# Kernel optimization log

Hardware: AMD Instinct MI355X
Metric: run time of the kernel (lower is better)

## Reference

```python
import jax, jax.numpy as jnp
import numpy as np

BIG = 1e9
EPS_BETA = 1e-6
EPS_BN = 1e-5

N_NODES = 50000
N_EDGES = 800000
IN_DIM = 128
OUT_DIM = 128


def setup_inputs() -> dict:
    key = jax.random.key(0)
    ks = jax.random.split(key, 8)
    h = jax.random.normal(ks[0], (N_NODES, IN_DIM), dtype=jnp.float32)
    src = jax.random.randint(ks[1], (N_EDGES,), 0, N_NODES, dtype=jnp.int32)
    dst = jax.random.randint(ks[2], (N_EDGES,), 0, N_NODES, dtype=jnp.int32)
    sigma_GD = jax.random.uniform(ks[3], (N_EDGES,), dtype=jnp.float32)
    fc_w = jax.random.normal(ks[4], (IN_DIM, OUT_DIM), dtype=jnp.float32) / np.sqrt(IN_DIM)
    fc_b = jax.random.normal(ks[5], (OUT_DIM,), dtype=jnp.float32) * 0.01
    attn_w = jax.random.normal(ks[6], (2 * OUT_DIM, 1), dtype=jnp.float32) / np.sqrt(2 * OUT_DIM)
    attn_b = jax.random.normal(ks[7], (1,), dtype=jnp.float32) * 0.01
    bn_gamma = jnp.ones((OUT_DIM,), dtype=jnp.float32)
    bn_beta = jnp.zeros((OUT_DIM,), dtype=jnp.float32)
    return {"h": h, "src": src, "dst": dst, "sigma_GD": sigma_GD,
            "fc_w": fc_w, "fc_b": fc_b, "attn_w": attn_w, "attn_b": attn_b,
            "bn_gamma": bn_gamma, "bn_beta": bn_beta}


def reference(h, src, dst, sigma_GD, fc_w, fc_b, attn_w, attn_b, bn_gamma, bn_beta):
    n = h.shape[0]
    # node projection
    z = h @ fc_w + fc_b                                   # [N, D]
    z = jnp.where(jnp.isinf(z), BIG, z)
    # per-edge attention logits: concat(src,dst) @ W == src@W1 + dst@W2 (avoid concat materialization)
    d = z.shape[1]
    w_src, w_dst = attn_w[:d], attn_w[d:]
    z_src = z[src]                                        # [E, D]
    a = z_src @ w_src + z[dst] @ w_dst + attn_b           # [E, 1]
    a = jnp.where(jnp.isinf(a), BIG, a)
    e = jax.nn.leaky_relu(a, negative_slope=0.01)[:, 0]   # [E]
    # segment softmax over incoming edges (mailbox softmax)
    m = jax.ops.segment_max(e, dst, num_segments=n)       # [N]
    ex = jnp.exp(e - m[dst])
    denom = jax.ops.segment_sum(ex, dst, num_segments=n)  # [N]
    alpha = ex / denom[dst]                               # [E]
    # beta: sigma_GD normalized per destination node
    bsum = jax.ops.segment_sum(sigma_GD, dst, num_segments=n)
    beta = sigma_GD / (bsum[dst] + EPS_BETA)              # [E]
    # weighted scatter-sum of source features
    h_new = jax.ops.segment_sum((alpha * beta)[:, None] * z_src, dst, num_segments=n)  # [N, D]
    h_new = jnp.where(jnp.isinf(h_new), BIG, h_new)
    # BatchNorm1d (training-mode batch stats, biased variance, as torch does)
    mu = h_new.mean(axis=0)
    var = ((h_new - mu) ** 2).mean(axis=0)
    h_bn = (h_new - mu) * jax.lax.rsqrt(var + EPS_BN) * bn_gamma + bn_beta
    return jax.nn.elu(h_bn)
```

## Files before the change

### kernel.cpp

```cpp
#include <hip/hip_runtime.h>
#include <hip/hip_fp16.h>
#include <math.h>

#define N_NODES 50000
#define N_EDGES 800000
#define BIGV 1000000000.0f
#define NBLK_SCAN 196
#define NBLK_GEMM 3125

typedef _Float16 half8 __attribute__((ext_vector_type(8)));
typedef float floatx4 __attribute__((ext_vector_type(4)));

__device__ __forceinline__ float clampinf(float x) { return isinf(x) ? BIGV : x; }

__device__ __forceinline__ void barrier_lgkm_only() {
    __builtin_amdgcn_sched_barrier(0);
    asm volatile("s_waitcnt lgkmcnt(0)" ::: "memory");
    __builtin_amdgcn_s_barrier();
    __builtin_amdgcn_sched_barrier(0);
}

__global__ __launch_bounds__(256) void k_wcast(const float* __restrict__ W,
                                               __half* __restrict__ wt,
                                               int* __restrict__ cnt,
                                               float* __restrict__ bns)
{
    int idx = blockIdx.x * 256 + threadIdx.x;
    int n = idx >> 7, k = idx & 127;
    wt[idx] = __float2half(W[k * 128 + n]);
    uint4 z; z.x = 0u; z.y = 0u; z.z = 0u; z.w = 0u;
    uint4* c4 = (uint4*)cnt;
    for (int i = idx; i < N_NODES * 4; i += 16384) c4[i] = z;
    if (idx < 256) bns[idx] = 0.f;
}

__global__ __launch_bounds__(256) void k_gemm(
    const float* __restrict__ h, const __half* __restrict__ wt,
    const float* __restrict__ bias, const float* __restrict__ attn_w,
    const int* __restrict__ dst, __half* __restrict__ zh,
    float* __restrict__ sv, float* __restrict__ tv,
    int* __restrict__ cnt, unsigned short* __restrict__ rank)
{
    __shared__ _Float16 hA[16][136];
    __shared__ float spart[4][16], tpart[4][16];

    const int tid = threadIdx.x;
    const int lane = tid & 63;
    const int wv = tid >> 6;
    const int l16 = lane & 15;
    const int oct = lane >> 4;
    const int n0 = wv << 5;
    const int node0 = blockIdx.x << 4;

    const int e = blockIdx.x * 256 + tid;
    const int d = dst[e];
    const int shard = blockIdx.x & 7;

    {
        const float4* h4 = (const float4*)(h + (size_t)node0 * 128);
        for (int i = tid; i < 512; i += 256) {
            int r = i >> 5, c4 = i & 31;
            float4 v = h4[i];
            union { __half2 h2[2]; uint2 u; } pk;
            pk.h2[0] = __floats2half2_rn(v.x, v.y);
            pk.h2[1] = __floats2half2_rn(v.z, v.w);
            *(uint2*)&hA[r][c4 << 2] = pk.u;
        }
    }

    half8 bfrag[4][2];
    #pragma unroll
    for (int kk = 0; kk < 4; ++kk)
        #pragma unroll
        for (int t = 0; t < 2; ++t)
            bfrag[kk][t] = *(const half8*)(wt + (size_t)(n0 + t * 16 + l16) * 128
                                              + kk * 32 + oct * 8);

    const float bv0 = bias[n0 + l16],         bv1 = bias[n0 + 16 + l16];
    const float ws0 = attn_w[n0 + l16],       ws1 = attn_w[n0 + 16 + l16];
    const float wd0 = attn_w[128 + n0 + l16], wd1 = attn_w[128 + n0 + 16 + l16];

    __builtin_amdgcn_sched_barrier(0);
    const int rk = atomicAdd(&cnt[(d << 4) + shard], 1);

    barrier_lgkm_only();

    floatx4 acc0 = {0.f, 0.f, 0.f, 0.f};
    floatx4 acc1 = {0.f, 0.f, 0.f, 0.f};
    #pragma unroll
    for (int kk = 0; kk < 4; ++kk) {
        half8 a = *(const half8*)&hA[l16][(kk << 5) + (oct << 3)];
        acc0 = __builtin_amdgcn_mfma_f32_16x16x32_f16(a, bfrag[kk][0], acc0, 0, 0, 0);
        acc1 = __builtin_amdgcn_mfma_f32_16x16x32_f16(a, bfrag[kk][1], acc1, 0, 0, 0);
    }

    float s_acc[4], t_acc[4];
    #pragma unroll
    for (int r = 0; r < 4; ++r) {
        float z0 = clampinf(acc0[r] + bv0);
        float z1 = clampinf(acc1[r] + bv1);
        const int row = (oct << 2) + r;
        zh[(size_t)(node0 + row) * 128 + n0 + l16]      = __float2half(z0);
        zh[(size_t)(node0 + row) * 128 + n0 + 16 + l16] = __float2half(z1);
        s_acc[r] = z0 * ws0 + z1 * ws1;
        t_acc[r] = z0 * wd0 + z1 * wd1;
    }
    #pragma unroll
    for (int r = 0; r < 4; ++r) {
        #pragma unroll
        for (int o = 1; o < 16; o <<= 1) {
            s_acc[r] += __shfl_xor(s_acc[r], o);
            t_acc[r] += __shfl_xor(t_acc[r], o);
        }
    }
    if (l16 == 0) {
        #pragma unroll
        for (int r = 0; r < 4; ++r) {
            spart[wv][(oct << 2) + r] = s_acc[r];
            tpart[wv][(oct << 2) + r] = t_acc[r];
        }
    }
    barrier_lgkm_only();
    if (tid < 16) {
        sv[node0 + tid] = spart[0][tid] + spart[1][tid] + spart[2][tid] + spart[3][tid];
        tv[node0 + tid] = tpart[0][tid] + tpart[1][tid] + tpart[2][tid] + tpart[3][tid];
    }
    rank[e] = (unsigned short)rk;
}

__global__ __launch_bounds__(256) void k_scan_bsum(int* __restrict__ cnt,
                                                   int* __restrict__ deg,
                                                   int* __restrict__ bsum)
{
    __shared__ int sdeg[256];
    const int t = threadIdx.x;
    const int idx = blockIdx.x * 256 + t;
    int dsum = 0;
    if (idx < N_NODES) {
        uint4* p = (uint4*)(cnt + ((size_t)idx << 4));
        uint4 a = p[0], b = p[1];
        unsigned e0 = 0;
        unsigned e1 = e0 + a.x;
        unsigned e2 = e1 + a.y;
        unsigned e3 = e2 + a.z;
        unsigned e4 = e3 + a.w;
        unsigned e5 = e4 + b.x;
        unsigned e6 = e5 + b.y;
        unsigned e7 = e6 + b.z;
        dsum = (int)(e7 + b.w);
        uint4 pa; pa.x = e0; pa.y = e1; pa.z = e2; pa.w = e3;
        uint4 pb; pb.x = e4; pb.y = e5; pb.z = e6; pb.w = e7;
        p[0] = pa; p[1] = pb;
        deg[idx] = dsum;
    }
    sdeg[t] = dsum;
    __syncthreads();
    for (int off = 128; off; off >>= 1) {
        if (t < off) sdeg[t] += sdeg[t + off];
        __syncthreads();
    }
    if (t == 0) bsum[blockIdx.x] = sdeg[0];
}

__global__ __launch_bounds__(256) void k_scan_final(const int* __restrict__ bsum,
                                                    const int* __restrict__ deg,
                                                    int* __restrict__ colptr)
{
    __shared__ int rs[256];
    __shared__ int s[256];
    const int t = threadIdx.x;

    int rv = (t < NBLK_SCAN) ? bsum[t] : 0;
    rs[t] = rv;
    __syncthreads();
    for (int off = 1; off < 256; off <<= 1) {
        int u = (t >= off) ? rs[t - off] : 0;
        __syncthreads();
        rs[t] += u;
        __syncthreads();
    }
    const int broot = (blockIdx.x > 0) ? rs[blockIdx.x - 1] : 0;
    if (blockIdx.x == 0 && t == 255) colptr[N_NODES] = rs[255];

    const int idx = blockIdx.x * 256 + t;
    int v = (idx < N_NODES) ? deg[idx] : 0;
    s[t] = v;
    __syncthreads();
    for (int off = 1; off < 256; off <<= 1) {
        int u = (t >= off) ? s[t - off] : 0;
        __syncthreads();
        s[t] += u;
        __syncthreads();
    }
    if (idx < N_NODES) colptr[idx] = broot + s[t] - v;
}

__global__ void k_scatter(const int* __restrict__ src, const int* __restrict__ dst,
                          const float* __restrict__ sigma,
                          const unsigned short* __restrict__ rank,
                          const int* __restrict__ colptr,
                          const int* __restrict__ cnt,
                          const float* __restrict__ sv, const float* __restrict__ tv,
                          const float* __restrict__ attn_b,
                          float4* __restrict__ recs)
{
    int e = blockIdx.x * 256 + threadIdx.x;
    if (e < N_EDGES) {
        int s = src[e];
        int d = dst[e];
        int shard = (e >> 8) & 7;
        float a = sv[s] + tv[d] + attn_b[0];
        a = clampinf(a);
        float ev = a > 0.f ? a : 0.01f * a;
        int pos = colptr[d] + cnt[(d << 4) + shard] + (int)rank[e];
        float4 rec;
        rec.x = __int_as_float(s);
        rec.y = sigma[e];
        rec.z = ev;
        rec.w = 0.f;
        recs[pos] = rec;
    }
}

__global__ __launch_bounds__(256) void k_agg(
    const int* __restrict__ colptr, const float4* __restrict__ recs,
    const __half* __restrict__ zh, float* __restrict__ out)
{
    const int lane = threadIdx.x & 63;
    const int node = blockIdx.x * 4 + (threadIdx.x >> 6);
    if (node >= N_NODES) return;
    const int base = colptr[node];
    const int deg = colptr[node + 1] - base;

    const int grp = lane >> 4;
    const int l16 = lane & 15;
    float acc[8] = {0.f, 0.f, 0.f, 0.f, 0.f, 0.f, 0.f, 0.f};

    if (deg > 0) {
        if (deg <= 64) {
            int sidx = 0; float sig = 0.f, e = -INFINITY;
            if (lane < deg) {
                float4 r = recs[base + lane];
                sidx = __float_as_int(r.x); sig = r.y; e = r.z;
            }
            float m = e;
            for (int o = 32; o; o >>= 1) m = fmaxf(m, __shfl_xor(m, o));
            float p = (lane < deg) ? __expf(e - m) : 0.f;
            float dn = p, bs = sig;
            for (int o = 32; o; o >>= 1) {
                dn += __shfl_xor(dn, o);
                bs += __shfl_xor(bs, o);
            }
            const float coef = p * sig * (1.0f / dn) / (bs + 1e-6f);
            for (int c = 0; c < deg; c += 4) {
                const int j = c + grp;
                const int js = (j < deg) ? j : 0;
                float cf = __shfl(coef, js);
                int sj = __shfl(sidx, js);
                if (j < deg) {
                    uint4 raw = *(const uint4*)(zh + ((size_t)sj << 7) + (l16 << 3));
                    const __half2* hp = (const __half2*)&raw;
                    #pragma unroll
                    for (int k = 0; k < 4; ++k) {
                        float2 f = __half22float2(hp[k]);
                        acc[2*k]   = fmaf(cf, f.x, acc[2*k]);
                        acc[2*k+1] = fmaf(cf, f.y, acc[2*k+1]);
                    }
                }
            }
        } else {
            float m = -INFINITY;
            for (int i = lane; i < deg; i += 64) m = fmaxf(m, recs[base + i].z);
            for (int o = 32; o; o >>= 1) m = fmaxf(m, __shfl_xor(m, o));
            float dn = 0.f, bs = 0.f;
            for (int i = lane; i < deg; i += 64) {
                float4 r = recs[base + i];
                dn += __expf(r.z - m); bs += r.y;
            }
            for (int o = 32; o; o >>= 1) {
                dn += __shfl_xor(dn, o);
                bs += __shfl_xor(bs, o);
            }
            const float scale = (1.0f / dn) / (bs + 1e-6f);
            for (int c = 0; c < deg; c += 64) {
                int i = c + lane;
                int sidx = 0; float coef = 0.f;
                if (i < deg) {
                    float4 r = recs[base + i];
                    sidx = __float_as_int(r.x);
                    coef = __expf(r.z - m) * r.y * scale;
                }
                const int cnt2 = min(64, deg - c);
                for (int j = 0; j < cnt2; j += 4) {
                    const int jj = j + grp;
                    const int js = (jj < cnt2) ? jj : 0;
                    float cf = __shfl(coef, js);
                    int sj = __shfl(sidx, js);
                    if (jj < cnt2) {
                        uint4 raw = *(const uint4*)(zh + ((size_t)sj << 7) + (l16 << 3));
                        const __half2* hp = (const __half2*)&raw;
                        #pragma unroll
                        for (int k = 0; k < 4; ++k) {
                            float2 f = __half22float2(hp[k]);
                            acc[2*k]   = fmaf(cf, f.x, acc[2*k]);
                            acc[2*k+1] = fmaf(cf, f.y, acc[2*k+1]);
                        }
                    }
                }
            }
        }
    }
    #pragma unroll
    for (int k = 0; k < 8; ++k) {
        acc[k] += __shfl_xor(acc[k], 16);
        acc[k] += __shfl_xor(acc[k], 32);
    }
    if (grp == 0) {
        float4 o0, o1;
        o0.x = clampinf(acc[0]); o0.y = clampinf(acc[1]);
        o0.z = clampinf(acc[2]); o0.w = clampinf(acc[3]);
        o1.x = clampinf(acc[4]); o1.y = clampinf(acc[5]);
        o1.z = clampinf(acc[6]); o1.w = clampinf(acc[7]);
        float4* op = (float4*)(out + (size_t)node * 128 + (l16 << 3));
        op[0] = o0; op[1] = o1;
    }
}

__global__ __launch_bounds__(256) void k_bnstats(const float* __restrict__ hnew,
                                                 float* __restrict__ sums)
{
    const int tid = threadIdx.x;
    const int f4 = (tid & 31) << 2;
    const int rgrp = tid >> 5;
    float4 s = {0.f, 0.f, 0.f, 0.f}, q = {0.f, 0.f, 0.f, 0.f};
    for (int node = blockIdx.x * 8 + rgrp; node < N_NODES; node += 256 * 8) {
        float4 v = *(const float4*)(hnew + (size_t)node * 128 + f4);
        s.x += v.x; s.y += v.y; s.z += v.z; s.w += v.w;
        q.x += v.x * v.x; q.y += v.y * v.y; q.z += v.z * v.z; q.w += v.w * v.w;
    }
    __shared__ float4 ls[256], lq[256];
    ls[tid] = s; lq[tid] = q;
    __syncthreads();
    for (int off = 128; off >= 32; off >>= 1) {
        if (tid < off) {
            float4 a = ls[tid + off], b = lq[tid + off];
            ls[tid].x += a.x; ls[tid].y += a.y; ls[tid].z += a.z; ls[tid].w += a.w;
            lq[tid].x += b.x; lq[tid].y += b.y; lq[tid].z += b.z; lq[tid].w += b.w;
        }
        __syncthreads();
    }
    if (tid < 32) {
        float4 fs = ls[tid], fq = lq[tid];
        atomicAdd(&sums[f4 + 0], fs.x);
        atomicAdd(&sums[f4 + 1], fs.y);
        atomicAdd(&sums[f4 + 2], fs.z);
        atomicAdd(&sums[f4 + 3], fs.w);
        atomicAdd(&sums[128 + f4 + 0], fq.x);
        atomicAdd(&sums[128 + f4 + 1], fq.y);
        atomicAdd(&sums[128 + f4 + 2], fq.z);
        atomicAdd(&sums[128 + f4 + 3], fq.w);
    }
}

__global__ __launch_bounds__(256) void k_bnapply(float* __restrict__ io,
                                                 const float* __restrict__ sums,
                                                 const float* __restrict__ gamma,
                                                 const float* __restrict__ beta)
{
    __shared__ float sc[128], sh[128];
    const int tid = threadIdx.x;
    if (tid < 128) {
        const float invn = 1.0f / (float)N_NODES;
        float mu = sums[tid] * invn;
        float var = fmaxf(sums[128 + tid] * invn - mu * mu, 0.f);
        float g = gamma[tid] * rsqrtf(var + 1e-5f);
        sc[tid] = g;
        sh[tid] = beta[tid] - mu * g;
    }
    __syncthreads();
    const size_t idx = (size_t)blockIdx.x * 256 + tid;
    const int f4 = ((int)idx & 31) << 2;
    float4 x = ((const float4*)io)[idx];
    float y0 = x.x * sc[f4 + 0] + sh[f4 + 0];
    float y1 = x.y * sc[f4 + 1] + sh[f4 + 1];
    float y2 = x.z * sc[f4 + 2] + sh[f4 + 2];
    float y3 = x.w * sc[f4 + 3] + sh[f4 + 3];
    float4 o;
    o.x = y0 > 0.f ? y0 : expm1f(y0);
    o.y = y1 > 0.f ? y1 : expm1f(y1);
    o.z = y2 > 0.f ? y2 : expm1f(y2);
    o.w = y3 > 0.f ? y3 : expm1f(y3);
    ((float4*)io)[idx] = o;
}

extern "C" void kernel_launch(void* const* d_in, const int* in_sizes, int n_in,
                              void* d_out, int out_size, void* d_ws, size_t ws_size,
                              hipStream_t stream)
{
    const float* h      = (const float*)d_in[0];
    const int*   src    = (const int*)  d_in[1];
    const int*   dst    = (const int*)  d_in[2];
    const float* sigma  = (const float*)d_in[3];
    const float* fc_w   = (const float*)d_in[4];
    const float* fc_b   = (const float*)d_in[5];
    const float* attn_w = (const float*)d_in[6];
    const float* attn_b = (const float*)d_in[7];
    const float* gamma  = (const float*)d_in[8];
    const float* beta   = (const float*)d_in[9];
    float* out = (float*)d_out;

    float4* recs   = (float4*)d_ws;
    __half* zh     = (__half*)(recs + N_EDGES);
    float*  sv     = (float*)(zh + (size_t)N_NODES * 128);
    float*  tv     = sv + N_NODES;
    float*  bns    = tv + N_NODES;
    int*    colptr = (int*)(bns + 256);
    int*    deg    = colptr + 50004;
    int*    bsum   = deg + N_NODES;
    int*    broot  = bsum + 256;
    __half* wt     = (__half*)(broot + 256);
    unsigned short* rank = (unsigned short*)(wt + 128 * 128);
    int*    cnt    = (int*)(rank + N_EDGES);

    k_wcast     <<<64, 256, 0, stream>>>(fc_w, wt, cnt, bns);
    k_gemm      <<<NBLK_GEMM, 256, 0, stream>>>(h, wt, fc_b, attn_w, dst,
                                                zh, sv, tv, cnt, rank);
    k_scan_bsum <<<NBLK_SCAN, 256, 0, stream>>>(cnt, deg, bsum);
    k_scan_final<<<NBLK_SCAN, 256, 0, stream>>>(bsum, deg, colptr);
    k_scatter   <<<N_EDGES / 256, 256, 0, stream>>>(src, dst, sigma, rank, colptr,
                                                    cnt, sv, tv, attn_b, recs);
    k_agg       <<<N_NODES / 4, 256, 0, stream>>>(colptr, recs, zh, out);
    k_bnstats   <<<256, 256, 0, stream>>>(out, bns);
    k_bnapply   <<<(N_NODES * 128) / (256 * 4), 256, 0, stream>>>(out, bns, gamma, beta);
}
```

Baseline: 232.9 us.

## Shard degree counters by XCC id with workgroup-scope atomics

Replaces the block-index-based shard for per-destination edge counters with the hardware XCC id read via s_getreg. Counters move to an XCC-major layout, and the atomic uses relaxed workgroup scope so it can resolve in the XCC-local L2 instead of going device-wide. The XCC id is packed into the upper bits of the 16-bit rank, and the scan and scatter kernels are updated to match. The approach relies on each XCC having its own coherent L2 so that workgroup-scope atomics on disjoint per-XCC counters stay correct. It also assumes per-XCC ranks fit in 12 bits.

```diff
diff --git a/kernel.cpp b/kernel.cpp
--- a/kernel.cpp
+++ b/kernel.cpp
@@ -7,6 +7,7 @@
 #define BIGV 1000000000.0f
 #define NBLK_SCAN 196
 #define NBLK_GEMM 3125
+#define CNT_STRIDE 50176
 
 typedef _Float16 half8 __attribute__((ext_vector_type(8)));
 typedef float floatx4 __attribute__((ext_vector_type(4)));
@@ -30,7 +31,7 @@
     wt[idx] = __float2half(W[k * 128 + n]);
     uint4 z; z.x = 0u; z.y = 0u; z.z = 0u; z.w = 0u;
     uint4* c4 = (uint4*)cnt;
-    for (int i = idx; i < N_NODES * 4; i += 16384) c4[i] = z;
+    for (int i = idx; i < (8 * CNT_STRIDE) / 4; i += 16384) c4[i] = z;
     if (idx < 256) bns[idx] = 0.f;
 }
 
@@ -54,7 +55,8 @@
 
     const int e = blockIdx.x * 256 + tid;
     const int d = dst[e];
-    const int shard = blockIdx.x & 7;
+    int xcc;
+    asm volatile("s_getreg_b32 %0, hwreg(HW_REG_XCC_ID)" : "=s"(xcc));
 
     {
         const float4* h4 = (const float4*)(h + (size_t)node0 * 128);
@@ -81,7 +83,9 @@
     const float wd0 = attn_w[128 + n0 + l16], wd1 = attn_w[128 + n0 + 16 + l16];
 
     __builtin_amdgcn_sched_barrier(0);
-    const int rk = atomicAdd(&cnt[(d << 4) + shard], 1);
+    const int rk = __hip_atomic_fetch_add(&cnt[xcc * CNT_STRIDE + d], 1,
+                                          __ATOMIC_RELAXED,
+                                          __HIP_MEMORY_SCOPE_WORKGROUP);
 
     barrier_lgkm_only();
 
@@ -125,7 +129,7 @@
         sv[node0 + tid] = spart[0][tid] + spart[1][tid] + spart[2][tid] + spart[3][tid];
         tv[node0 + tid] = tpart[0][tid] + tpart[1][tid] + tpart[2][tid] + tpart[3][tid];
     }
-    rank[e] = (unsigned short)rk;
+    rank[e] = (unsigned short)((xcc << 12) | rk);
 }
 
 __global__ __launch_bounds__(256) void k_scan_bsum(int* __restrict__ cnt,
@@ -137,20 +141,17 @@
     const int idx = blockIdx.x * 256 + t;
     int dsum = 0;
     if (idx < N_NODES) {
-        uint4* p = (uint4*)(cnt + ((size_t)idx << 4));
-        uint4 a = p[0], b = p[1];
-        unsigned e0 = 0;
-        unsigned e1 = e0 + a.x;
-        unsigned e2 = e1 + a.y;
-        unsigned e3 = e2 + a.z;
-        unsigned e4 = e3 + a.w;
-        unsigned e5 = e4 + b.x;
-        unsigned e6 = e5 + b.y;
-        unsigned e7 = e6 + b.z;
-        dsum = (int)(e7 + b.w);
-        uint4 pa; pa.x = e0; pa.y = e1; pa.z = e2; pa.w = e3;
-        uint4 pb; pb.x = e4; pb.y = e5; pb.z = e6; pb.w = e7;
-        p[0] = pa; p[1] = pb;
+        int c[8];
+        #pragma unroll
+        for (int s = 0; s < 8; ++s) c[s] = cnt[s * CNT_STRIDE + idx];
+        int run = 0;
+        #pragma unroll
+        for (int s = 0; s < 8; ++s) {
+            int v = c[s];
+            cnt[s * CNT_STRIDE + idx] = run;
+            run += v;
+        }
+        dsum = run;
         deg[idx] = dsum;
     }
     sdeg[t] = dsum;
@@ -208,11 +209,13 @@
     if (e < N_EDGES) {
         int s = src[e];
         int d = dst[e];
-        int shard = (e >> 8) & 7;
+        unsigned rr = rank[e];
+        int xcc = rr >> 12;
+        int rk  = rr & 4095;
         float a = sv[s] + tv[d] + attn_b[0];
         a = clampinf(a);
         float ev = a > 0.f ? a : 0.01f * a;
-        int pos = colptr[d] + cnt[(d << 4) + shard] + (int)rank[e];
+        int pos = colptr[d] + cnt[xcc * CNT_STRIDE + d] + rk;
         float4 rec;
         rec.x = __int_as_float(s);
         rec.y = sigma[e];
```

New measurement: 226.2 us. 1.03x faster.
